# Kernel optimization log

Hardware: AMD Instinct MI355X
Metric: run time of the kernel (lower is better)

The kernel has to match this reference:

```python
import jax, jax.numpy as jnp
import numpy as np

B, T, E = 1, 4096, 1024
H = 16
D = E // H  # head_dim = 64


def setup_inputs() -> dict:
    key = jax.random.key(0)
    k1, k2, k3 = jax.random.split(key, 3)
    x = jax.random.normal(k1, (B, T, E), dtype=jnp.float32)
    w_qkv = jax.random.normal(k2, (E, 3 * E), dtype=jnp.float32) * (1.0 / np.sqrt(E))
    b_qkv = jnp.zeros((3 * E,), dtype=jnp.float32)
    w_out = jax.random.normal(k3, (E, E), dtype=jnp.float32) * (1.0 / np.sqrt(E))
    b_out = jnp.zeros((E,), dtype=jnp.float32)
    return {"x": x, "w_qkv": w_qkv, "b_qkv": b_qkv, "w_out": w_out, "b_out": b_out}


def reference(x, w_qkv, b_qkv, w_out, b_out):
    b, t, e = x.shape
    scale = 1.0 / np.sqrt(D)
    qkv = x @ w_qkv + b_qkv                      # [b, t, 3e]
    q, k, v = jnp.split(qkv, 3, axis=-1)
    # [b, h, t, d]
    q = q.reshape(b, t, H, D).transpose(0, 2, 1, 3)
    k = k.reshape(b, t, H, D).transpose(0, 2, 1, 3)
    v = v.reshape(b, t, H, D).transpose(0, 2, 1, 3)
    attn = jnp.einsum("bhqd,bhkd->bhqk", q, k) * scale  # [b, h, t, t]
    causal = jnp.tril(jnp.ones((t, t), dtype=bool))
    attn = jnp.where(causal, attn, -jnp.inf)
    attn = jax.nn.softmax(attn, axis=-1)
    out = jnp.einsum("bhqk,bhkd->bhqd", attn, v)        # [b, h, t, d]
    out = out.transpose(0, 2, 1, 3).reshape(b, t, e)
    return out @ w_out + b_out
```

## Files before the change

### kernel.cpp

```cpp
#include <hip/hip_runtime.h>
#include <hip/hip_bf16.h>


#define T_SEQ 4096
#define EMB   1024
#define NH    16
#define HD    64
#define N_QKV 3072

typedef __bf16 bf16x8 __attribute__((ext_vector_type(8)));
typedef __bf16 bf16x4 __attribute__((ext_vector_type(4)));
typedef float  f32x4  __attribute__((ext_vector_type(4)));

__device__ inline f32x4 mfma16(bf16x8 a, bf16x8 b, f32x4 c) {
    return __builtin_amdgcn_mfma_f32_16x16x32_bf16(a, b, c, 0, 0, 0);
}

__device__ inline void async_copy16(const void* g, void* l) {
    __builtin_amdgcn_global_load_lds(
        (const __attribute__((address_space(1))) unsigned int*)g,
        (__attribute__((address_space(3))) unsigned int*)l, 16, 0, 0);
}

__device__ inline bf16x8 lds_read8(const __bf16* base, int row, int colByte) {
    return *(const bf16x8*)((const char*)base + row * 128 +
                            (colByte ^ ((row & 7) << 4)));
}

__global__ __launch_bounds__(256) void f32_to_bf16_kernel(const float* __restrict__ in,
                                                          __bf16* __restrict__ out, int n) {
    int i = (blockIdx.x * 256 + threadIdx.x) * 4;
    if (i >= n) return;
    float4 v = *(const float4*)&in[i];
    bf16x4 o;
    o[0] = (__bf16)v.x; o[1] = (__bf16)v.y; o[2] = (__bf16)v.z; o[3] = (__bf16)v.w;
    *(bf16x4*)&out[i] = o;
}

__global__ __launch_bounds__(256) void transpose_to_bf16_kernel(const float* __restrict__ in,
                                                                __bf16* __restrict__ out,
                                                                int K, int N) {
    __shared__ __bf16 tl[32][33];
    int k0 = blockIdx.x * 32, n0 = blockIdx.y * 32;
    int t = threadIdx.x;
    int r = t >> 3, c4 = (t & 7) * 4;
    float4 v = *(const float4*)&in[(size_t)(k0 + r) * N + n0 + c4];
    tl[r][c4 + 0] = (__bf16)v.x;
    tl[r][c4 + 1] = (__bf16)v.y;
    tl[r][c4 + 2] = (__bf16)v.z;
    tl[r][c4 + 3] = (__bf16)v.w;
    __syncthreads();
    bf16x4 o;
    o[0] = tl[c4 + 0][r];
    o[1] = tl[c4 + 1][r];
    o[2] = tl[c4 + 2][r];
    o[3] = tl[c4 + 3][r];
    *(bf16x4*)&out[(size_t)(n0 + r) * K + k0 + c4] = o;
}

__global__ __launch_bounds__(256) void gemm_qkv_kernel(const __bf16* __restrict__ A,
                                                       const __bf16* __restrict__ Bt,
                                                       const float* __restrict__ bias,
                                                       __bf16* __restrict__ Qo,
                                                       __bf16* __restrict__ Ko,
                                                       __bf16* __restrict__ Vo) {
    const int K = EMB;
    int m0 = blockIdx.y * 128, n0 = blockIdx.x * 128;
    int tid = threadIdx.x;
    int w = tid >> 6, l = tid & 63, lg = l >> 4, lr = l & 15;
    int wr = w >> 1, wc = w & 1;

    __shared__ __align__(16) __bf16 As[128 * 32];
    __shared__ __align__(16) __bf16 Bs[128 * 32];

    f32x4 acc[4][4];
#pragma unroll
    for (int mi = 0; mi < 4; ++mi)
#pragma unroll
        for (int ni = 0; ni < 4; ++ni) acc[mi][ni] = (f32x4){0.f, 0.f, 0.f, 0.f};

    for (int k0 = 0; k0 < K; k0 += 32) {
        __syncthreads();
#pragma unroll
        for (int i = 0; i < 2; ++i) {
            int flat = tid + 256 * i;
            int row = flat >> 2, c = flat & 3;
            async_copy16(&A[(size_t)(m0 + row) * K + k0 + c * 8], As + flat * 8);
            async_copy16(&Bt[(size_t)(n0 + row) * K + k0 + c * 8], Bs + flat * 8);
        }
        __syncthreads();
        bf16x8 af[4], bfr[4];
#pragma unroll
        for (int mi = 0; mi < 4; ++mi) af[mi] = *(const bf16x8*)(As + (wr * 64 + mi * 16 + lr) * 32 + lg * 8);
#pragma unroll
        for (int ni = 0; ni < 4; ++ni) bfr[ni] = *(const bf16x8*)(Bs + (wc * 64 + ni * 16 + lr) * 32 + lg * 8);
#pragma unroll
        for (int mi = 0; mi < 4; ++mi)
#pragma unroll
            for (int ni = 0; ni < 4; ++ni)
                acc[mi][ni] = mfma16(af[mi], bfr[ni], acc[mi][ni]);
    }

    const float QSC = 0.18033688011112042f;
#pragma unroll
    for (int mi = 0; mi < 4; ++mi) {
#pragma unroll
        for (int ni = 0; ni < 4; ++ni) {
            int n = n0 + wc * 64 + ni * 16 + lr;
            float bv = bias[n];
            int mat = n >> 10, rem = n & 1023, hh = rem >> 6, d = rem & 63;
#pragma unroll
            for (int r = 0; r < 4; ++r) {
                int mr = m0 + wr * 64 + mi * 16 + lg * 4 + r;
                float v = acc[mi][ni][r] + bv;
                size_t idx = ((size_t)hh * T_SEQ + mr) * HD + d;
                if (mat == 0)      Qo[idx] = (__bf16)(v * QSC);
                else if (mat == 1) Ko[idx] = (__bf16)v;
                else               Vo[idx] = (__bf16)v;
            }
        }
    }
}

__global__ __launch_bounds__(256) void vt_kernel(const __bf16* __restrict__ V,
                                                 __bf16* __restrict__ VT) {
    __shared__ __bf16 tl[64][72];
    int h = blockIdx.y, t0 = blockIdx.x * 64;
    int tid = threadIdx.x;
    const __bf16* Vh = V + (size_t)h * T_SEQ * HD;
#pragma unroll
    for (int i = 0; i < 2; ++i) {
        int flat = tid + 256 * i;
        int r = flat >> 3, sl = flat & 7;
        *(bf16x8*)&tl[r][sl * 8] = *(const bf16x8*)&Vh[(size_t)(t0 + r) * HD + sl * 8];
    }
    __syncthreads();
    __bf16* VTh = VT + (size_t)h * HD * T_SEQ;
#pragma unroll
    for (int i = 0; i < 2; ++i) {
        int flat = tid + 256 * i;
        int d = flat >> 3, sl = flat & 7;
        bf16x8 o;
#pragma unroll
        for (int j = 0; j < 8; ++j) o[j] = tl[sl * 8 + j][d];
        *(bf16x8*)&VTh[(size_t)d * T_SEQ + t0 + sl * 8] = o;
    }
}

__global__ __launch_bounds__(512) void attn_kernel(const __bf16* __restrict__ Qg,
                                                   const __bf16* __restrict__ Kg,
                                                   const __bf16* __restrict__ VTg,
                                                   __bf16* __restrict__ Og) {
    __shared__ __align__(16) __bf16 Ks[2][64 * 64];
    __shared__ __align__(16) __bf16 Vs[2][64 * 64];
    __shared__ __align__(16) __bf16 Ps[8][16 * 64];

    const int bid = blockIdx.x;
    const int xcd = bid & 7, li = bid >> 3;
    const int h = xcd * 2 + (li & 1);
    const int bx = 31 - (li >> 1);
    const int qb = bx * 128;
    const int tid = threadIdx.x;
    const int w = tid >> 6, l = tid & 63, lg = l >> 4, lr = l & 15;
    const int qr0 = qb + 16 * w;

    const __bf16* Qh = Qg + (size_t)h * T_SEQ * HD;
    const __bf16* Kh = Kg + (size_t)h * T_SEQ * HD;
    const __bf16* Vh = VTg + (size_t)h * HD * T_SEQ;
    __bf16* PsW = &Ps[w][0];

    const int srow = tid >> 3, sslot = tid & 7;
    const int sB = (sslot * 16) ^ ((srow & 7) << 4);
    const size_t kOff = (size_t)srow * HD + (sB >> 1);
    const size_t vOff = (size_t)srow * T_SEQ + (sB >> 1);

    bf16x8 qf[2];
#pragma unroll
    for (int kd = 0; kd < 2; ++kd)
        qf[kd] = *(const bf16x8*)&Qh[(size_t)(qr0 + lr) * HD + kd * 32 + lg * 8];

    f32x4 oacc[4];
#pragma unroll
    for (int n = 0; n < 4; ++n) oacc[n] = (f32x4){0.f, 0.f, 0.f, 0.f};
    float m = -1e30f, lsum = 0.f;

    const int ntiles = 2 * bx + 2;

    async_copy16(Kh + kOff, &Ks[0][tid * 8]);
    async_copy16(Vh + vOff, &Vs[0][tid * 8]);
    __syncthreads();

    int cur = 0;
    for (int t = 0; t < ntiles; ++t) {
        const int kv0 = t * 64;
        if (t + 1 < ntiles) {
            async_copy16(Kh + (size_t)(t + 1) * 64 * HD + kOff, &Ks[cur ^ 1][tid * 8]);
            async_copy16(Vh + (size_t)(t + 1) * 64 + vOff, &Vs[cur ^ 1][tid * 8]);
        }
        if (kv0 <= qr0 + 15) {
            const __bf16* Ksc = &Ks[cur][0];
            const __bf16* Vsc = &Vs[cur][0];

            bf16x8 kf[4][2];
#pragma unroll
            for (int blk = 0; blk < 4; ++blk)
#pragma unroll
                for (int kd = 0; kd < 2; ++kd)
                    kf[blk][kd] = lds_read8(Ksc, blk * 16 + lr, kd * 64 + lg * 16);

            __builtin_amdgcn_s_setprio(1);
            f32x4 s[4];
#pragma unroll
            for (int blk = 0; blk < 4; ++blk) {
                f32x4 a = (f32x4){0.f, 0.f, 0.f, 0.f};
                a = mfma16(kf[blk][0], qf[0], a);
                a = mfma16(kf[blk][1], qf[1], a);
                s[blk] = a;
            }
            __builtin_amdgcn_s_setprio(0);

            float mx = -1e30f;
            if (kv0 + 63 > qr0) {
#pragma unroll
                for (int blk = 0; blk < 4; ++blk)
#pragma unroll
                    for (int r = 0; r < 4; ++r) {
                        int kv = kv0 + 16 * blk + 4 * lg + r;
                        float sv = (kv <= qr0 + lr) ? s[blk][r] : -1e30f;
                        s[blk][r] = sv;
                        mx = fmaxf(mx, sv);
                    }
            } else {
#pragma unroll
                for (int blk = 0; blk < 4; ++blk)
#pragma unroll
                    for (int r = 0; r < 4; ++r) mx = fmaxf(mx, s[blk][r]);
            }
            mx = fmaxf(mx, __shfl_xor(mx, 16, 64));
            mx = fmaxf(mx, __shfl_xor(mx, 32, 64));

            if (!__all(mx <= m + 8.f)) {
                float mnew = fmaxf(m, mx);
                float alpha = exp2f(m - mnew);
                m = mnew;
                lsum *= alpha;
                float ar[4];
#pragma unroll
                for (int r = 0; r < 4; ++r) ar[r] = __shfl(alpha, 4 * lg + r, 64);
#pragma unroll
                for (int n = 0; n < 4; ++n)
#pragma unroll
                    for (int r = 0; r < 4; ++r) oacc[n][r] *= ar[r];
            }

            float ps = 0.f;
            char* pw = (char*)PsW + lr * 128;
            const int swz = (lr & 7) << 4;
#pragma unroll
            for (int blk = 0; blk < 4; ++blk) {
                bf16x4 pk;
#pragma unroll
                for (int r = 0; r < 4; ++r) {
                    float p = exp2f(s[blk][r] - m);
                    ps += p;
                    pk[r] = (__bf16)p;
                }
                *(bf16x4*)(pw + ((32 * blk + 8 * lg) ^ swz)) = pk;
            }
            ps += __shfl_xor(ps, 16, 64);
            ps += __shfl_xor(ps, 32, 64);
            lsum += ps;

            __builtin_amdgcn_s_setprio(1);
#pragma unroll
            for (int kc = 0; kc < 2; ++kc) {
                bf16x8 pa = lds_read8(PsW, lr, kc * 64 + lg * 16);
#pragma unroll
                for (int n = 0; n < 4; ++n) {
                    bf16x8 vb = lds_read8(Vsc, 16 * n + lr, kc * 64 + lg * 16);
                    oacc[n] = mfma16(pa, vb, oacc[n]);
                }
            }
            __builtin_amdgcn_s_setprio(0);
        }
        __syncthreads();
        cur ^= 1;
    }

    float linv = 1.0f / lsum;
    float lrv[4];
#pragma unroll
    for (int r = 0; r < 4; ++r) lrv[r] = __shfl(linv, 4 * lg + r, 64);
#pragma unroll
    for (int n = 0; n < 4; ++n)
#pragma unroll
        for (int r = 0; r < 4; ++r) {
            int q = qr0 + 4 * lg + r;
            Og[(size_t)q * EMB + h * HD + 16 * n + lr] = (__bf16)(oacc[n][r] * lrv[r]);
        }
}

__global__ __launch_bounds__(256) void gemm_out_kernel(const __bf16* __restrict__ A,
                                                       const __bf16* __restrict__ Bt,
                                                       const float* __restrict__ bias,
                                                       float* __restrict__ out) {
    const int K = EMB;
    int m0 = blockIdx.y * 128, n0 = blockIdx.x * 128;
    int tid = threadIdx.x;
    int w = tid >> 6, l = tid & 63, lg = l >> 4, lr = l & 15;
    int wr = w >> 1, wc = w & 1;

    __shared__ __align__(16) __bf16 As[128 * 32];
    __shared__ __align__(16) __bf16 Bs[128 * 32];

    f32x4 acc[4][4];
#pragma unroll
    for (int mi = 0; mi < 4; ++mi)
#pragma unroll
        for (int ni = 0; ni < 4; ++ni) acc[mi][ni] = (f32x4){0.f, 0.f, 0.f, 0.f};

    for (int k0 = 0; k0 < K; k0 += 32) {
        __syncthreads();
#pragma unroll
        for (int i = 0; i < 2; ++i) {
            int flat = tid + 256 * i;
            int row = flat >> 2, c = flat & 3;
            async_copy16(&A[(size_t)(m0 + row) * K + k0 + c * 8], As + flat * 8);
            async_copy16(&Bt[(size_t)(n0 + row) * K + k0 + c * 8], Bs + flat * 8);
        }
        __syncthreads();
        bf16x8 af[4], bfr[4];
#pragma unroll
        for (int mi = 0; mi < 4; ++mi) af[mi] = *(const bf16x8*)(As + (wr * 64 + mi * 16 + lr) * 32 + lg * 8);
#pragma unroll
        for (int ni = 0; ni < 4; ++ni) bfr[ni] = *(const bf16x8*)(Bs + (wc * 64 + ni * 16 + lr) * 32 + lg * 8);
#pragma unroll
        for (int mi = 0; mi < 4; ++mi)
#pragma unroll
            for (int ni = 0; ni < 4; ++ni)
                acc[mi][ni] = mfma16(af[mi], bfr[ni], acc[mi][ni]);
    }

#pragma unroll
    for (int mi = 0; mi < 4; ++mi) {
#pragma unroll
        for (int ni = 0; ni < 4; ++ni) {
            int n = n0 + wc * 64 + ni * 16 + lr;
            float bv = bias[n];
#pragma unroll
            for (int r = 0; r < 4; ++r) {
                int mr = m0 + wr * 64 + mi * 16 + lg * 4 + r;
                out[(size_t)mr * EMB + n] = acc[mi][ni][r] + bv;
            }
        }
    }
}

extern "C" void kernel_launch(void* const* d_in, const int* in_sizes, int n_in,
                              void* d_out, int out_size, void* d_ws, size_t ws_size,
                              hipStream_t stream) {
    const float* x      = (const float*)d_in[0];
    const float* w_qkv  = (const float*)d_in[1];
    const float* b_qkv  = (const float*)d_in[2];
    const float* w_out  = (const float*)d_in[3];
    const float* b_out  = (const float*)d_in[4];
    float* out = (float*)d_out;

    char* ws = (char*)d_ws;
    __bf16* xb    = (__bf16*)(ws);
    __bf16* AO    = (__bf16*)(ws);
    __bf16* wqkvT = (__bf16*)(ws + ((size_t)8 << 20));
    __bf16* woutT = (__bf16*)(ws + ((size_t)14 << 20));
    __bf16* Qh    = (__bf16*)(ws + ((size_t)16 << 20));
    __bf16* Kh    = (__bf16*)(ws + ((size_t)24 << 20));
    __bf16* Vh    = (__bf16*)(ws + ((size_t)32 << 20));
    __bf16* VTh   = (__bf16*)(ws + ((size_t)40 << 20));

    f32_to_bf16_kernel<<<dim3(T_SEQ * EMB / (256 * 4)), 256, 0, stream>>>(x, xb, T_SEQ * EMB);
    transpose_to_bf16_kernel<<<dim3(EMB / 32, N_QKV / 32), 256, 0, stream>>>(w_qkv, wqkvT, EMB, N_QKV);
    transpose_to_bf16_kernel<<<dim3(EMB / 32, EMB / 32), 256, 0, stream>>>(w_out, woutT, EMB, EMB);

    gemm_qkv_kernel<<<dim3(N_QKV / 128, T_SEQ / 128), 256, 0, stream>>>(xb, wqkvT, b_qkv, Qh, Kh, Vh);

    vt_kernel<<<dim3(T_SEQ / 64, NH), 256, 0, stream>>>(Vh, VTh);

    attn_kernel<<<dim3(512), 512, 0, stream>>>(Qh, Kh, VTh, AO);

    gemm_out_kernel<<<dim3(EMB / 128, T_SEQ / 128), 256, 0, stream>>>(AO, woutT, b_out, out);
}
```

Baseline: 246.5 us.

## Merge prep kernels and halve attention query tile to 64 rows

The three conversion/transpose launches are merged into one prep kernel dispatched by block index, removing two kernel launches. The attention kernel moves from 128-query blocks of 512 threads to 64-query blocks of 256 threads, doubling the grid to 1024 blocks. Each thread now issues two async copies per K and V tile, and the per-warp causal skip is dropped. Blocks are ordered to pair long and short causal rows for load balance, at the cost of less K/V reuse per block.

```diff
diff --git a/kernel.cpp b/kernel.cpp
--- a/kernel.cpp
+++ b/kernel.cpp
@@ -27,22 +27,29 @@
                             (colByte ^ ((row & 7) << 4)));
 }
 
-__global__ __launch_bounds__(256) void f32_to_bf16_kernel(const float* __restrict__ in,
-                                                          __bf16* __restrict__ out, int n) {
-    int i = (blockIdx.x * 256 + threadIdx.x) * 4;
-    if (i >= n) return;
-    float4 v = *(const float4*)&in[i];
-    bf16x4 o;
-    o[0] = (__bf16)v.x; o[1] = (__bf16)v.y; o[2] = (__bf16)v.z; o[3] = (__bf16)v.w;
-    *(bf16x4*)&out[i] = o;
-}
-
-__global__ __launch_bounds__(256) void transpose_to_bf16_kernel(const float* __restrict__ in,
-                                                                __bf16* __restrict__ out,
-                                                                int K, int N) {
+__global__ __launch_bounds__(256) void prep_kernel(const float* __restrict__ x,
+                                                   const float* __restrict__ w_qkv,
+                                                   const float* __restrict__ w_out,
+                                                   __bf16* __restrict__ xb,
+                                                   __bf16* __restrict__ wqkvT,
+                                                   __bf16* __restrict__ woutT) {
     __shared__ __bf16 tl[32][33];
-    int k0 = blockIdx.x * 32, n0 = blockIdx.y * 32;
+    int b = blockIdx.x;
     int t = threadIdx.x;
+    if (b < 4096) {
+        int i = (b * 256 + t) * 4;
+        float4 v = *(const float4*)&x[i];
+        bf16x4 o;
+        o[0] = (__bf16)v.x; o[1] = (__bf16)v.y; o[2] = (__bf16)v.z; o[3] = (__bf16)v.w;
+        *(bf16x4*)&xb[i] = o;
+        return;
+    }
+    const float* in;
+    __bf16* out;
+    int N, bb;
+    if (b < 7168) { bb = b - 4096; in = w_qkv; out = wqkvT; N = N_QKV; }
+    else          { bb = b - 7168; in = w_out; out = woutT; N = EMB; }
+    int k0 = (bb & 31) * 32, n0 = (bb >> 5) * 32;
     int r = t >> 3, c4 = (t & 7) * 4;
     float4 v = *(const float4*)&in[(size_t)(k0 + r) * N + n0 + c4];
     tl[r][c4 + 0] = (__bf16)v.x;
@@ -55,7 +62,7 @@
     o[1] = tl[c4 + 1][r];
     o[2] = tl[c4 + 2][r];
     o[3] = tl[c4 + 3][r];
-    *(bf16x4*)&out[(size_t)(n0 + r) * K + k0 + c4] = o;
+    *(bf16x4*)&out[(size_t)(n0 + r) * EMB + k0 + c4] = o;
 }
 
 __global__ __launch_bounds__(256) void gemm_qkv_kernel(const __bf16* __restrict__ A,
@@ -147,19 +154,20 @@
     }
 }
 
-__global__ __launch_bounds__(512) void attn_kernel(const __bf16* __restrict__ Qg,
+__global__ __launch_bounds__(256) void attn_kernel(const __bf16* __restrict__ Qg,
                                                    const __bf16* __restrict__ Kg,
                                                    const __bf16* __restrict__ VTg,
                                                    __bf16* __restrict__ Og) {
     __shared__ __align__(16) __bf16 Ks[2][64 * 64];
     __shared__ __align__(16) __bf16 Vs[2][64 * 64];
-    __shared__ __align__(16) __bf16 Ps[8][16 * 64];
+    __shared__ __align__(16) __bf16 Ps[4][16 * 64];
 
     const int bid = blockIdx.x;
     const int xcd = bid & 7, li = bid >> 3;
     const int h = xcd * 2 + (li & 1);
-    const int bx = 31 - (li >> 1);
-    const int qb = bx * 128;
+    const int j = li >> 1;
+    const int bx = (j < 32) ? (63 - j) : (j - 32);
+    const int qb = bx * 64;
     const int tid = threadIdx.x;
     const int w = tid >> 6, l = tid & 63, lg = l >> 4, lr = l & 15;
     const int qr0 = qb + 16 * w;
@@ -171,8 +179,10 @@
 
     const int srow = tid >> 3, sslot = tid & 7;
     const int sB = (sslot * 16) ^ ((srow & 7) << 4);
-    const size_t kOff = (size_t)srow * HD + (sB >> 1);
-    const size_t vOff = (size_t)srow * T_SEQ + (sB >> 1);
+    const size_t kOff0 = (size_t)srow * HD + (sB >> 1);
+    const size_t kOff1 = kOff0 + (size_t)32 * HD;
+    const size_t vOff0 = (size_t)srow * T_SEQ + (sB >> 1);
+    const size_t vOff1 = vOff0 + (size_t)32 * T_SEQ;
 
     bf16x8 qf[2];
 #pragma unroll
@@ -184,20 +194,26 @@
     for (int n = 0; n < 4; ++n) oacc[n] = (f32x4){0.f, 0.f, 0.f, 0.f};
     float m = -1e30f, lsum = 0.f;
 
-    const int ntiles = 2 * bx + 2;
-
-    async_copy16(Kh + kOff, &Ks[0][tid * 8]);
-    async_copy16(Vh + vOff, &Vs[0][tid * 8]);
+    const int ntiles = bx + 1;
+
+    async_copy16(Kh + kOff0, &Ks[0][tid * 8]);
+    async_copy16(Kh + kOff1, &Ks[0][(tid + 256) * 8]);
+    async_copy16(Vh + vOff0, &Vs[0][tid * 8]);
+    async_copy16(Vh + vOff1, &Vs[0][(tid + 256) * 8]);
     __syncthreads();
 
     int cur = 0;
     for (int t = 0; t < ntiles; ++t) {
         const int kv0 = t * 64;
         if (t + 1 < ntiles) {
-            async_copy16(Kh + (size_t)(t + 1) * 64 * HD + kOff, &Ks[cur ^ 1][tid * 8]);
-            async_copy16(Vh + (size_t)(t + 1) * 64 + vOff, &Vs[cur ^ 1][tid * 8]);
-        }
-        if (kv0 <= qr0 + 15) {
+            const size_t kb = (size_t)(t + 1) * 64 * HD;
+            const size_t vb = (size_t)(t + 1) * 64;
+            async_copy16(Kh + kb + kOff0, &Ks[cur ^ 1][tid * 8]);
+            async_copy16(Kh + kb + kOff1, &Ks[cur ^ 1][(tid + 256) * 8]);
+            async_copy16(Vh + vb + vOff0, &Vs[cur ^ 1][tid * 8]);
+            async_copy16(Vh + vb + vOff1, &Vs[cur ^ 1][(tid + 256) * 8]);
+        }
+        {
             const __bf16* Ksc = &Ks[cur][0];
             const __bf16* Vsc = &Vs[cur][0];
 
@@ -376,15 +392,13 @@
     __bf16* Vh    = (__bf16*)(ws + ((size_t)32 << 20));
     __bf16* VTh   = (__bf16*)(ws + ((size_t)40 << 20));
 
-    f32_to_bf16_kernel<<<dim3(T_SEQ * EMB / (256 * 4)), 256, 0, stream>>>(x, xb, T_SEQ * EMB);
-    transpose_to_bf16_kernel<<<dim3(EMB / 32, N_QKV / 32), 256, 0, stream>>>(w_qkv, wqkvT, EMB, N_QKV);
-    transpose_to_bf16_kernel<<<dim3(EMB / 32, EMB / 32), 256, 0, stream>>>(w_out, woutT, EMB, EMB);
+    prep_kernel<<<dim3(8192), 256, 0, stream>>>(x, w_qkv, w_out, xb, wqkvT, woutT);
 
     gemm_qkv_kernel<<<dim3(N_QKV / 128, T_SEQ / 128), 256, 0, stream>>>(xb, wqkvT, b_qkv, Qh, Kh, Vh);
 
     vt_kernel<<<dim3(T_SEQ / 64, NH), 256, 0, stream>>>(Vh, VTh);
 
-    attn_kernel<<<dim3(512), 512, 0, stream>>>(Qh, Kh, VTh, AO);
+    attn_kernel<<<dim3(1024), 256, 0, stream>>>(Qh, Kh, VTh, AO);
 
     gemm_out_kernel<<<dim3(EMB / 128, T_SEQ / 128), 256, 0, stream>>>(AO, woutT, b_out, out);
 }
```

Measured after the change: 231.9 us. 1.06x faster.
